# Performance work log

Hardware: AMD Instinct MI355X
Metric: run time of the kernel (lower is better)

The kernel has to match this reference:

```python
import jax, jax.numpy as jnp
import numpy as np

NUM_ITERS = 10
G_KSIZE, G_SIGMA = 5, 0.5
BIL_KSIZE, BIL_SIG_COLOR, BIL_SIG_SPACE = 5, 0.5, 5.0
EDGE_KSIZE, EDGE_SIG_COLOR, EDGE_SIG_SPACE = 5, 0.5, 5.0


def _gauss1d(ksize, sigma):
    x = jnp.arange(ksize, dtype=jnp.float32) - ksize // 2  # odd ksize -> centered (kornia)
    g = jnp.exp(-(x * x) / (2.0 * sigma * sigma))
    return g / g.sum()


def gaussian_blur(q, ksize, sigma):
    # separable gaussian blur with reflect padding, kornia GaussianBlur2d semantics
    k = _gauss1d(ksize, sigma)
    r = ksize // 2
    B, C, H, W = q.shape
    qp = jnp.pad(q, ((0, 0), (0, 0), (r, r), (0, 0)), mode='reflect')
    q = sum(k[i] * qp[:, :, i:i + H, :] for i in range(ksize))
    qp = jnp.pad(q, ((0, 0), (0, 0), (0, 0), (r, r)), mode='reflect')
    q = sum(k[i] * qp[:, :, :, i:i + W] for i in range(ksize))
    return q


def bilateral_weights(guide, ksize, sigma_color, sigma_space):
    # kornia joint_bilateral_blur weights (l1 color distance, reflect border).
    # guide: [B, Cg, H, W] -> weights [B, K*K, H, W]; guidance is constant across
    # CRF iterations so we precompute the kernel once.
    B, Cg, H, W = guide.shape
    r = ksize // 2
    g1 = _gauss1d(ksize, sigma_space)
    space = jnp.outer(g1, g1)  # normalized 2d gaussian (kornia get_gaussian_kernel2d)
    gp = jnp.pad(guide, ((0, 0), (0, 0), (r, r), (r, r)), mode='reflect')
    inv2sc2 = -0.5 / (sigma_color * sigma_color)
    ws = []
    for dy in range(ksize):
        for dx in range(ksize):
            d = jnp.abs(gp[:, :, dy:dy + H, dx:dx + W] - guide).sum(axis=1)  # [B,H,W]
            ws.append(space[dy, dx] * jnp.exp(inv2sc2 * d * d))
    return jnp.stack(ws, axis=1)  # [B, K*K, H, W]


def bilateral_apply(q, weights, ksize):
    # q: [B,C,H,W], weights: [B,K*K,H,W]
    B, C, H, W = q.shape
    r = ksize // 2
    qp = jnp.pad(q, ((0, 0), (0, 0), (r, r), (r, r)), mode='reflect')
    num = jnp.zeros_like(q)
    idx = 0
    for dy in range(ksize):
        for dx in range(ksize):
            num = num + weights[:, idx][:, None] * qp[:, :, dy:dy + H, dx:dx + W]
            idx += 1
    den = weights.sum(axis=1)[:, None]  # [B,1,H,W]
    return num / den


def _compat(f):
    # compat matrix is -1 off-diagonal, 0 on diagonal:
    # pairwise[c] = -sum_{c'!=c} f[c'] = f[c] - sum_{c'} f[c']
    return f - f.sum(axis=1, keepdims=True)


def setup_inputs() -> dict:
    key = jax.random.key(0)
    k1, k2, k3 = jax.random.split(key, 3)
    B, C, H, W = 2, 21, 512, 512
    unary_logits = jax.random.normal(k1, (B, C, H, W), dtype=jnp.float32)
    image = jax.random.uniform(k2, (B, 3, H, W), dtype=jnp.float32)
    edges = jax.random.uniform(k3, (B, H, W), dtype=jnp.float32)
    return {"unary_logits": unary_logits, "image": image, "edges": edges}


def reference(unary_logits, image, edges):
    edges4 = edges[:, None]  # [B,1,H,W]
    w_rgb = bilateral_weights(image, BIL_KSIZE, BIL_SIG_COLOR, BIL_SIG_SPACE)
    w_edge = bilateral_weights(edges4, EDGE_KSIZE, EDGE_SIG_COLOR, EDGE_SIG_SPACE)
    q = jax.nn.softmax(unary_logits, axis=1)
    for _ in range(NUM_ITERS):
        sf = gaussian_blur(q, G_KSIZE, G_SIGMA)
        rf = bilateral_apply(q, w_rgb, BIL_KSIZE)
        ef = bilateral_apply(q, w_edge, EDGE_KSIZE)
        pairwise = _compat(sf) + _compat(rf) + _compat(ef)
        q = jax.nn.softmax(unary_logits - pairwise, axis=1)
    return q
```

## Files before the change

### kernel.cpp

```cpp
#include <hip/hip_runtime.h>
#include <math.h>

#define BATCH 2
#define NCH 21
#define CPAD 24
#define WUPAD 48
#define HH 512
#define WW 512
#define KS 5
#define RAD 2
#define NTAPS 25
#define NUM_ITERS 10

#define TXW 32
#define TYW 16
#define HXW (TXW + 2*RAD)
#define HYW (TYW + 2*RAD)
#define HPXW (HXW * HYW)

#define TW 32
#define TH 16
#define NTHR 512
#define SX 40
#define SY 24
#define SPX (SX * SY)
#define SCHUNK (SPX * 3)
#define EX 36
#define EY 20
#define EPX (EX * EY)
#define RING (EPX - TW*TH)

typedef _Float16 f16;
typedef _Float16 half8 __attribute__((ext_vector_type(8)));
typedef _Float16 half2v __attribute__((ext_vector_type(2)));

__device__ __forceinline__ int refl(int i, int n) {
    if (i < 0) i = -i;
    if (i >= n) i = 2*n - 2 - i;
    return i;
}

#define WSEL(h0, h1, h2, hl, t) \
    ((t) < 8 ? (h0)[(t)] : (t) < 16 ? (h1)[(t) - 8] : (t) < 24 ? (h2)[(t) - 16] : (hl))

__global__ __launch_bounds__(512) void setup_kernel(const float* __restrict__ image,
                                                    const float* __restrict__ edges,
                                                    const float* __restrict__ unary,
                                                    f16* __restrict__ wu,
                                                    f16* __restrict__ q) {
    __shared__ __align__(16) float4 spx[HYW][HXW];

    const int tx = threadIdx.x;
    const int ty = threadIdx.y;
    const int tid = ty * TXW + tx;
    const int x0 = blockIdx.x * TXW;
    const int y0 = blockIdx.y * TYW;
    const int b = blockIdx.z;
    const int x = x0 + tx;
    const int y = y0 + ty;
    const size_t plane = (size_t)HH * WW;
    const float* img = image + (size_t)b * 3 * plane;
    const float* edg = edges + (size_t)b * plane;

    for (int i = tid; i < HPXW; i += TXW * TYW) {
        int ly = i / HXW, lx = i - ly * HXW;
        int gy = refl(y0 + ly - RAD, HH);
        int gx = refl(x0 + lx - RAD, WW);
        int g = gy * WW + gx;
        float4 v;
        v.x = img[g];
        v.y = img[plane + g];
        v.z = img[2 * plane + g];
        v.w = edg[g];
        spx[ly][lx] = v;
    }

    float l[NCH];
    {
        const float* u = unary + (size_t)b * NCH * plane + (size_t)y * WW + x;
#pragma unroll
        for (int c = 0; c < NCH; c++) l[c] = u[c * plane];
    }

    __syncthreads();

    float gs[3];
    gs[0] = 1.0f; gs[1] = __expf(-1.0f / 50.0f); gs[2] = __expf(-4.0f / 50.0f);
    float gb[3];
    gb[0] = 1.0f; gb[1] = __expf(-2.0f); gb[2] = __expf(-8.0f);
    float gbs = gb[0] + 2.0f * (gb[1] + gb[2]);
    gb[0] /= gbs; gb[1] /= gbs; gb[2] /= gbs;

    const float4 c0 = spx[ty + RAD][tx + RAD];
    const float r0 = c0.x, g0 = c0.y, b0 = c0.z, e0 = c0.w;

    float wr[NTAPS], we[NTAPS];
    float sr = 0.f, se = 0.f;
#pragma unroll
    for (int dy = 0; dy < KS; dy++) {
#pragma unroll
        for (int dx = 0; dx < KS; dx++) {
            float sp = gs[abs(dy - RAD)] * gs[abs(dx - RAD)];
            float4 v = spx[ty + dy][tx + dx];
            float d = fabsf(v.x - r0)
                    + fabsf(v.y - g0)
                    + fabsf(v.z - b0);
            float w1 = sp * __expf(-2.0f * d * d);
            float de = fabsf(v.w - e0);
            float w2 = sp * __expf(-2.0f * de * de);
            wr[dy * KS + dx] = w1;
            we[dy * KS + dx] = w2;
            sr += w1;
            se += w2;
        }
    }
    float isr = 1.0f / sr, ise = 1.0f / se;
    float wt[NTAPS];
#pragma unroll
    for (int t = 0; t < NTAPS; t++) {
        int dy = t / KS, dx = t % KS;
        float g2 = gb[abs(dy - RAD)] * gb[abs(dx - RAD)];
        wt[t] = g2 + wr[t] * isr + we[t] * ise;
    }
    const size_t pixoff = (size_t)b * plane + (size_t)y * WW + x;

    {
        half8* wo = (half8*)(wu + pixoff * WUPAD);
        half8 v;
#pragma unroll
        for (int k = 0; k < 8; k++) v[k] = (f16)wt[k];
        wo[0] = v;
#pragma unroll
        for (int k = 0; k < 8; k++) v[k] = (f16)wt[8 + k];
        wo[1] = v;
#pragma unroll
        for (int k = 0; k < 8; k++) v[k] = (f16)wt[16 + k];
        wo[2] = v;
#pragma unroll
        for (int k = 0; k < 8; k++) v[k] = (f16)l[k];
        wo[3] = v;
#pragma unroll
        for (int k = 0; k < 8; k++) v[k] = (f16)l[8 + k];
        wo[4] = v;
#pragma unroll
        for (int k = 0; k < 5; k++) v[k] = (f16)l[16 + k];
        v[5] = (f16)wt[24];
        v[6] = (f16)0.f; v[7] = (f16)0.f;
        wo[5] = v;
    }

    {
        float m = l[0];
#pragma unroll
        for (int c = 1; c < NCH; c++) m = fmaxf(m, l[c]);
        float e[NCH];
        float s = 0.f;
#pragma unroll
        for (int c = 0; c < NCH; c++) { e[c] = __expf(l[c] - m); s += e[c]; }
        float is = 1.0f / s;
        half8* qo = (half8*)(q + pixoff * CPAD);
        half8 v;
#pragma unroll
        for (int k = 0; k < 8; k++) v[k] = (f16)(e[k] * is);
        qo[0] = v;
#pragma unroll
        for (int k = 0; k < 8; k++) v[k] = (f16)(e[8 + k] * is);
        qo[1] = v;
#pragma unroll
        for (int k = 0; k < 5; k++) v[k] = (f16)(e[16 + k] * is);
        v[5] = (f16)0.f; v[6] = (f16)0.f; v[7] = (f16)0.f;
        qo[2] = v;
    }
}

#define CONV_ACC_PK(acc2, lds, row0, col0, stride, W0, W1, W2, WL)                     \
    {                                                                                  \
        _Pragma("unroll")                                                              \
        for (int dy = 0; dy < KS; dy++) {                                              \
            _Pragma("unroll")                                                          \
            for (int dx = 0; dx < KS; dx++) {                                          \
                const f16 wt_ = WSEL(W0, W1, W2, WL, dy * KS + dx);                    \
                const half2v wv_ = {wt_, wt_};                                         \
                const f16* tp = (lds) + ((size_t)((row0) + dy) * (stride) + (col0) + dx) * CPAD; \
                half8 v0 = *(const half8*)(tp);                                        \
                half8 v1 = *(const half8*)(tp + 8);                                    \
                half8 v2 = *(const half8*)(tp + 16);                                   \
                acc2[0]  = __builtin_elementwise_fma(wv_, __builtin_shufflevector(v0, v0, 0, 1), acc2[0]);  \
                acc2[1]  = __builtin_elementwise_fma(wv_, __builtin_shufflevector(v0, v0, 2, 3), acc2[1]);  \
                acc2[2]  = __builtin_elementwise_fma(wv_, __builtin_shufflevector(v0, v0, 4, 5), acc2[2]);  \
                acc2[3]  = __builtin_elementwise_fma(wv_, __builtin_shufflevector(v0, v0, 6, 7), acc2[3]);  \
                acc2[4]  = __builtin_elementwise_fma(wv_, __builtin_shufflevector(v1, v1, 0, 1), acc2[4]);  \
                acc2[5]  = __builtin_elementwise_fma(wv_, __builtin_shufflevector(v1, v1, 2, 3), acc2[5]);  \
                acc2[6]  = __builtin_elementwise_fma(wv_, __builtin_shufflevector(v1, v1, 4, 5), acc2[6]);  \
                acc2[7]  = __builtin_elementwise_fma(wv_, __builtin_shufflevector(v1, v1, 6, 7), acc2[7]);  \
                acc2[8]  = __builtin_elementwise_fma(wv_, __builtin_shufflevector(v2, v2, 0, 1), acc2[8]);  \
                acc2[9]  = __builtin_elementwise_fma(wv_, __builtin_shufflevector(v2, v2, 2, 3), acc2[9]);  \
                acc2[10] = __builtin_elementwise_fma(wv_, __builtin_shufflevector(v2, v2, 4, 5), acc2[10]); \
            }                                                                          \
        }                                                                              \
    }

#define LOGITS_FROM_PK(l, acc2, U0, U1, U2)                                            \
    {                                                                                  \
        _Pragma("unroll")                                                              \
        for (int j = 0; j < 10; j++) {                                                 \
            l[2 * j]     = -(float)acc2[j][0];                                         \
            l[2 * j + 1] = -(float)acc2[j][1];                                         \
        }                                                                              \
        l[20] = -(float)acc2[10][0];                                                   \
        _Pragma("unroll")                                                              \
        for (int k = 0; k < 8; k++) l[k] += (float)U0[k];                              \
        _Pragma("unroll")                                                              \
        for (int k = 0; k < 8; k++) l[8 + k] += (float)U1[k];                          \
        _Pragma("unroll")                                                              \
        for (int k = 0; k < 5; k++) l[16 + k] += (float)U2[k];                         \
    }

template <bool FINAL>
__global__ __launch_bounds__(NTHR, 4) void crf_pair_kernel(const f16* __restrict__ qin,
                                                           const f16* __restrict__ wu,
                                                           void* __restrict__ qout) {
    __shared__ __align__(16) f16 buf[SPX][CPAD];

    const int tid = threadIdx.x;
    const int ix = tid & (TW - 1);
    const int iy = tid >> 5;

    const int flat = blockIdx.x;
    const int band = flat & 7;
    const int within = flat >> 3;
    const int b = within >> 6;
    const int r = within & 63;
    const int x0 = (r & 15) * TW;
    const int y0 = (band * 4 + (r >> 4)) * TH;
    const int gx = x0 + ix;
    const int gy = y0 + iy;
    const size_t plane = (size_t)HH * WW;

    const f16* qbase = qin + (size_t)b * plane * CPAD;
    f16* lbase = &buf[0][0];
    for (int idx = tid; idx < SCHUNK; idx += NTHR) {
        int px = idx / 3, h4 = idx - px * 3;
        int sly = px / SX, slx = px - sly * SX;
        int qy = refl(y0 - 4 + sly, HH);
        int qx = refl(x0 - 4 + slx, WW);
        const f16* g = qbase + ((size_t)(qy * WW + qx)) * CPAD + h4 * 8;
        __builtin_amdgcn_global_load_lds(
            (const __attribute__((address_space(1))) void*)g,
            (__attribute__((address_space(3))) void*)(lbase + (size_t)idx * 8),
            16, 0, 0);
    }

    const size_t pixoff = (size_t)b * plane + (size_t)gy * WW + gx;
    const half8* wp = (const half8*)(wu + pixoff * WUPAD);
    half8 wa0 = wp[0], wa1 = wp[1], wa2 = wp[2];
    half8 ui0 = wp[3], ui1 = wp[4], ui2 = wp[5];
    f16 wl = ui2[5];

    const bool has_ring = tid < RING;
    int rly = 0, rlx = 0;
    half8 wr0 = {}, wr1 = {}, wr2 = {}, ur0 = {}, ur1 = {}, ur2 = {};
    f16 wrl = (f16)0.f;
    if (has_ring) {
        int t = tid;
        if (t < 72)       { rly = t / 36;       rlx = t % 36; }
        else if (t < 144) { t -= 72;  rly = 18 + t / 36; rlx = t % 36; }
        else              { t -= 144; rly = 2 + (t >> 2); int c = t & 3; rlx = (c < 2) ? c : (c + 32); }
        int rgy = y0 + rly - 2, rgx = x0 + rlx - 2;
        int cy = min(max(rgy, 0), HH - 1);
        int cx = min(max(rgx, 0), WW - 1);
        size_t rpo = (size_t)b * plane + (size_t)cy * WW + cx;
        const half8* wpr = (const half8*)(wu + rpo * WUPAD);
        wr0 = wpr[0]; wr1 = wpr[1]; wr2 = wpr[2];
        ur0 = wpr[3]; ur1 = wpr[4]; ur2 = wpr[5];
        wrl = ur2[5];
    }

    __syncthreads();

    half8 qr0, qr1, qr2;
    if (has_ring) {
        half2v acc2[11];
#pragma unroll
        for (int j = 0; j < 11; j++) acc2[j] = (half2v){(f16)0.f, (f16)0.f};
        CONV_ACC_PK(acc2, lbase, rly, rlx, SX, wr0, wr1, wr2, wrl);
        float l[NCH];
        LOGITS_FROM_PK(l, acc2, ur0, ur1, ur2);
        float m = l[0];
#pragma unroll
        for (int c = 1; c < NCH; c++) m = fmaxf(m, l[c]);
        float s = 0.f;
#pragma unroll
        for (int c = 0; c < NCH; c++) { l[c] = __expf(l[c] - m); s += l[c]; }
        float is = 1.0f / s;
#pragma unroll
        for (int k = 0; k < 8; k++) qr0[k] = (f16)(l[k] * is);
#pragma unroll
        for (int k = 0; k < 8; k++) qr1[k] = (f16)(l[8 + k] * is);
#pragma unroll
        for (int k = 0; k < 5; k++) qr2[k] = (f16)(l[16 + k] * is);
        qr2[5] = (f16)0.f; qr2[6] = (f16)0.f; qr2[7] = (f16)0.f;
    }

    half8 qi0, qi1, qi2;
    {
        half2v acc2[11];
#pragma unroll
        for (int j = 0; j < 11; j++) acc2[j] = (half2v){(f16)0.f, (f16)0.f};
        CONV_ACC_PK(acc2, lbase, iy + 2, ix + 2, SX, wa0, wa1, wa2, wl);
        float l[NCH];
        LOGITS_FROM_PK(l, acc2, ui0, ui1, ui2);
        float m = l[0];
#pragma unroll
        for (int c = 1; c < NCH; c++) m = fmaxf(m, l[c]);
        float s = 0.f;
#pragma unroll
        for (int c = 0; c < NCH; c++) { l[c] = __expf(l[c] - m); s += l[c]; }
        float is = 1.0f / s;
#pragma unroll
        for (int k = 0; k < 8; k++) qi0[k] = (f16)(l[k] * is);
#pragma unroll
        for (int k = 0; k < 8; k++) qi1[k] = (f16)(l[8 + k] * is);
#pragma unroll
        for (int k = 0; k < 5; k++) qi2[k] = (f16)(l[16 + k] * is);
        qi2[5] = (f16)0.f; qi2[6] = (f16)0.f; qi2[7] = (f16)0.f;
    }

    __syncthreads();

    {
        half8* d = (half8*)(lbase + ((size_t)(iy + 2) * EX + (ix + 2)) * CPAD);
        d[0] = qi0; d[1] = qi1; d[2] = qi2;
        if (has_ring) {
            half8* dr = (half8*)(lbase + ((size_t)rly * EX + rlx) * CPAD);
            dr[0] = qr0; dr[1] = qr1; dr[2] = qr2;
        }
    }

    __syncthreads();

    {
        int ry[KS], rx[KS];
#pragma unroll
        for (int d = 0; d < KS; d++) {
            ry[d] = refl(gy + d - 2, HH) - (y0 - 2);
            rx[d] = refl(gx + d - 2, WW) - (x0 - 2);
        }
        half2v acc2[11];
#pragma unroll
        for (int j = 0; j < 11; j++) acc2[j] = (half2v){(f16)0.f, (f16)0.f};
#pragma unroll
        for (int dy = 0; dy < KS; dy++) {
#pragma unroll
            for (int dx = 0; dx < KS; dx++) {
                const f16 wt_ = WSEL(wa0, wa1, wa2, wl, dy * KS + dx);
                const half2v wv_ = {wt_, wt_};
                const f16* tp = lbase + ((size_t)ry[dy] * EX + rx[dx]) * CPAD;
                half8 v0 = *(const half8*)(tp);
                half8 v1 = *(const half8*)(tp + 8);
                half8 v2 = *(const half8*)(tp + 16);
                acc2[0]  = __builtin_elementwise_fma(wv_, __builtin_shufflevector(v0, v0, 0, 1), acc2[0]);
                acc2[1]  = __builtin_elementwise_fma(wv_, __builtin_shufflevector(v0, v0, 2, 3), acc2[1]);
                acc2[2]  = __builtin_elementwise_fma(wv_, __builtin_shufflevector(v0, v0, 4, 5), acc2[2]);
                acc2[3]  = __builtin_elementwise_fma(wv_, __builtin_shufflevector(v0, v0, 6, 7), acc2[3]);
                acc2[4]  = __builtin_elementwise_fma(wv_, __builtin_shufflevector(v1, v1, 0, 1), acc2[4]);
                acc2[5]  = __builtin_elementwise_fma(wv_, __builtin_shufflevector(v1, v1, 2, 3), acc2[5]);
                acc2[6]  = __builtin_elementwise_fma(wv_, __builtin_shufflevector(v1, v1, 4, 5), acc2[6]);
                acc2[7]  = __builtin_elementwise_fma(wv_, __builtin_shufflevector(v1, v1, 6, 7), acc2[7]);
                acc2[8]  = __builtin_elementwise_fma(wv_, __builtin_shufflevector(v2, v2, 0, 1), acc2[8]);
                acc2[9]  = __builtin_elementwise_fma(wv_, __builtin_shufflevector(v2, v2, 2, 3), acc2[9]);
                acc2[10] = __builtin_elementwise_fma(wv_, __builtin_shufflevector(v2, v2, 4, 5), acc2[10]);
            }
        }
        float l[NCH];
        LOGITS_FROM_PK(l, acc2, ui0, ui1, ui2);
        float m = l[0];
#pragma unroll
        for (int c = 1; c < NCH; c++) m = fmaxf(m, l[c]);
        float s = 0.f;
#pragma unroll
        for (int c = 0; c < NCH; c++) { l[c] = __expf(l[c] - m); s += l[c]; }
        float is = 1.0f / s;

        if (FINAL) {
            float* qo = (float*)qout + (size_t)b * NCH * plane + (size_t)gy * WW + gx;
#pragma unroll
            for (int c = 0; c < NCH; c++) qo[c * plane] = l[c] * is;
        } else {
            half8* qo = (half8*)((f16*)qout + pixoff * CPAD);
            half8 o0, o1, o2;
#pragma unroll
            for (int k = 0; k < 8; k++) o0[k] = (f16)(l[k] * is);
#pragma unroll
            for (int k = 0; k < 8; k++) o1[k] = (f16)(l[8 + k] * is);
#pragma unroll
            for (int k = 0; k < 5; k++) o2[k] = (f16)(l[16 + k] * is);
            o2[5] = (f16)0.f; o2[6] = (f16)0.f; o2[7] = (f16)0.f;
            qo[0] = o0; qo[1] = o1; qo[2] = o2;
        }
    }
}

extern "C" void kernel_launch(void* const* d_in, const int* in_sizes, int n_in,
                              void* d_out, int out_size, void* d_ws, size_t ws_size,
                              hipStream_t stream) {
    const float* unary = (const float*)d_in[0];
    const float* image = (const float*)d_in[1];
    const float* edges = (const float*)d_in[2];
    float* out = (float*)d_out;

    const size_t plane = (size_t)HH * WW;
    char* ws = (char*)d_ws;
    f16* wu = (f16*)ws;
    char* p1 = ws + sizeof(f16) * BATCH * plane * WUPAD;
    f16* qA = (f16*)p1;
    f16* qB = qA + (size_t)BATCH * plane * CPAD;

    dim3 gridW(WW / TXW, HH / TYW, BATCH);
    dim3 blockW(TXW, TYW, 1);
    setup_kernel<<<gridW, blockW, 0, stream>>>(image, edges, unary, wu, qA);

    const int nblk = (WW / TW) * (HH / TH) * BATCH;
    f16* qa = qA;
    f16* qb = qB;
    const int npairs = NUM_ITERS / 2;
    for (int it = 0; it < npairs - 1; it++) {
        crf_pair_kernel<false><<<nblk, NTHR, 0, stream>>>(qa, wu, (void*)qb);
        f16* t = qa; qa = qb; qb = t;
    }
    crf_pair_kernel<true><<<nblk, NTHR, 0, stream>>>(qa, wu, (void*)out);
}
```

Baseline: 284.6 us.

## Add dedicated ring warps so halo softmax runs alongside inner pixels

The fused two-iteration kernel grows from 512 to 640 threads per block. The extra two warps compute the halo-ring pixels, two per thread, while the original 512 threads only compute their inner pixel. Before, the first 208 threads did the ring pixel and then their inner pixel serially. This removes that imbalance at the cost of more threads per block and a lower occupancy bound (3 blocks per CU instead of 4).

```diff
diff --git a/kernel.cpp b/kernel.cpp
--- a/kernel.cpp
+++ b/kernel.cpp
@@ -20,7 +20,8 @@
 
 #define TW 32
 #define TH 16
-#define NTHR 512
+#define NTHR 640
+#define NINNER 512
 #define SX 40
 #define SY 24
 #define SPX (SX * SY)
@@ -38,6 +39,12 @@
     if (i < 0) i = -i;
     if (i >= n) i = 2*n - 2 - i;
     return i;
+}
+
+__device__ __forceinline__ void ring_map(int t, int& rly, int& rlx) {
+    if (t < 72)       { rly = t / 36;            rlx = t % 36; }
+    else if (t < 144) { t -= 72;  rly = 18 + t / 36; rlx = t % 36; }
+    else              { t -= 144; rly = 2 + (t >> 2); int c = t & 3; rlx = (c < 2) ? c : (c + 32); }
 }
 
 #define WSEL(h0, h1, h2, hl, t) \
@@ -216,8 +223,32 @@
         for (int k = 0; k < 5; k++) l[16 + k] += (float)U2[k];                         \
     }
 
+#define CONV_SOFTMAX(o0, o1, o2, row0, col0, W0, W1, W2, WL, U0, U1, U2)               \
+    {                                                                                  \
+        half2v acc2[11];                                                               \
+        _Pragma("unroll")                                                              \
+        for (int j = 0; j < 11; j++) acc2[j] = (half2v){(f16)0.f, (f16)0.f};           \
+        CONV_ACC_PK(acc2, lbase, row0, col0, SX, W0, W1, W2, WL);                      \
+        float l_[NCH];                                                                 \
+        LOGITS_FROM_PK(l_, acc2, U0, U1, U2);                                          \
+        float m_ = l_[0];                                                              \
+        _Pragma("unroll")                                                              \
+        for (int c = 1; c < NCH; c++) m_ = fmaxf(m_, l_[c]);                           \
+        float s_ = 0.f;                                                                \
+        _Pragma("unroll")                                                              \
+        for (int c = 0; c < NCH; c++) { l_[c] = __expf(l_[c] - m_); s_ += l_[c]; }     \
+        float is_ = 1.0f / s_;                                                         \
+        _Pragma("unroll")                                                              \
+        for (int k = 0; k < 8; k++) (o0)[k] = (f16)(l_[k] * is_);                      \
+        _Pragma("unroll")                                                              \
+        for (int k = 0; k < 8; k++) (o1)[k] = (f16)(l_[8 + k] * is_);                  \
+        _Pragma("unroll")                                                              \
+        for (int k = 0; k < 5; k++) (o2)[k] = (f16)(l_[16 + k] * is_);                 \
+        (o2)[5] = (f16)0.f; (o2)[6] = (f16)0.f; (o2)[7] = (f16)0.f;                    \
+    }
+
 template <bool FINAL>
-__global__ __launch_bounds__(NTHR, 4) void crf_pair_kernel(const f16* __restrict__ qin,
+__global__ __launch_bounds__(NTHR, 3) void crf_pair_kernel(const f16* __restrict__ qin,
                                                            const f16* __restrict__ wu,
                                                            void* __restrict__ qout) {
     __shared__ __align__(16) f16 buf[SPX][CPAD];
@@ -225,6 +256,7 @@
     const int tid = threadIdx.x;
     const int ix = tid & (TW - 1);
     const int iy = tid >> 5;
+    const bool is_inner = tid < NINNER;
 
     const int flat = blockIdx.x;
     const int band = flat & 7;
@@ -252,94 +284,78 @@
     }
 
     const size_t pixoff = (size_t)b * plane + (size_t)gy * WW + gx;
-    const half8* wp = (const half8*)(wu + pixoff * WUPAD);
-    half8 wa0 = wp[0], wa1 = wp[1], wa2 = wp[2];
-    half8 ui0 = wp[3], ui1 = wp[4], ui2 = wp[5];
-    f16 wl = ui2[5];
-
-    const bool has_ring = tid < RING;
-    int rly = 0, rlx = 0;
-    half8 wr0 = {}, wr1 = {}, wr2 = {}, ur0 = {}, ur1 = {}, ur2 = {};
-    f16 wrl = (f16)0.f;
-    if (has_ring) {
-        int t = tid;
-        if (t < 72)       { rly = t / 36;       rlx = t % 36; }
-        else if (t < 144) { t -= 72;  rly = 18 + t / 36; rlx = t % 36; }
-        else              { t -= 144; rly = 2 + (t >> 2); int c = t & 3; rlx = (c < 2) ? c : (c + 32); }
-        int rgy = y0 + rly - 2, rgx = x0 + rlx - 2;
-        int cy = min(max(rgy, 0), HH - 1);
-        int cx = min(max(rgx, 0), WW - 1);
-        size_t rpo = (size_t)b * plane + (size_t)cy * WW + cx;
-        const half8* wpr = (const half8*)(wu + rpo * WUPAD);
-        wr0 = wpr[0]; wr1 = wpr[1]; wr2 = wpr[2];
-        ur0 = wpr[3]; ur1 = wpr[4]; ur2 = wpr[5];
-        wrl = ur2[5];
+    half8 wa0 = {}, wa1 = {}, wa2 = {}, ui0 = {}, ui1 = {}, ui2 = {};
+    f16 wl = (f16)0.f;
+    if (is_inner) {
+        const half8* wp = (const half8*)(wu + pixoff * WUPAD);
+        wa0 = wp[0]; wa1 = wp[1]; wa2 = wp[2];
+        ui0 = wp[3]; ui1 = wp[4]; ui2 = wp[5];
+        wl = ui2[5];
+    }
+
+    int rlyA = 0, rlxA = 0, rlyB = 0, rlxB = 0;
+    bool has_rB = false;
+    half8 wrA0 = {}, wrA1 = {}, wrA2 = {}, urA0 = {}, urA1 = {}, urA2 = {};
+    half8 wrB0 = {}, wrB1 = {}, wrB2 = {}, urB0 = {}, urB1 = {}, urB2 = {};
+    f16 wrlA = (f16)0.f, wrlB = (f16)0.f;
+    if (!is_inner) {
+        int j = tid - NINNER;
+        ring_map(j, rlyA, rlxA);
+        {
+            int rgy = y0 + rlyA - 2, rgx = x0 + rlxA - 2;
+            int cy = min(max(rgy, 0), HH - 1);
+            int cx = min(max(rgx, 0), WW - 1);
+            size_t rpo = (size_t)b * plane + (size_t)cy * WW + cx;
+            const half8* wpr = (const half8*)(wu + rpo * WUPAD);
+            wrA0 = wpr[0]; wrA1 = wpr[1]; wrA2 = wpr[2];
+            urA0 = wpr[3]; urA1 = wpr[4]; urA2 = wpr[5];
+            wrlA = urA2[5];
+        }
+        has_rB = (j < RING - 128);
+        if (has_rB) {
+            ring_map(128 + j, rlyB, rlxB);
+            int rgy = y0 + rlyB - 2, rgx = x0 + rlxB - 2;
+            int cy = min(max(rgy, 0), HH - 1);
+            int cx = min(max(rgx, 0), WW - 1);
+            size_t rpo = (size_t)b * plane + (size_t)cy * WW + cx;
+            const half8* wpr = (const half8*)(wu + rpo * WUPAD);
+            wrB0 = wpr[0]; wrB1 = wpr[1]; wrB2 = wpr[2];
+            urB0 = wpr[3]; urB1 = wpr[4]; urB2 = wpr[5];
+            wrlB = urB2[5];
+        }
     }
 
     __syncthreads();
 
-    half8 qr0, qr1, qr2;
-    if (has_ring) {
-        half2v acc2[11];
-#pragma unroll
-        for (int j = 0; j < 11; j++) acc2[j] = (half2v){(f16)0.f, (f16)0.f};
-        CONV_ACC_PK(acc2, lbase, rly, rlx, SX, wr0, wr1, wr2, wrl);
-        float l[NCH];
-        LOGITS_FROM_PK(l, acc2, ur0, ur1, ur2);
-        float m = l[0];
-#pragma unroll
-        for (int c = 1; c < NCH; c++) m = fmaxf(m, l[c]);
-        float s = 0.f;
-#pragma unroll
-        for (int c = 0; c < NCH; c++) { l[c] = __expf(l[c] - m); s += l[c]; }
-        float is = 1.0f / s;
-#pragma unroll
-        for (int k = 0; k < 8; k++) qr0[k] = (f16)(l[k] * is);
-#pragma unroll
-        for (int k = 0; k < 8; k++) qr1[k] = (f16)(l[8 + k] * is);
-#pragma unroll
-        for (int k = 0; k < 5; k++) qr2[k] = (f16)(l[16 + k] * is);
-        qr2[5] = (f16)0.f; qr2[6] = (f16)0.f; qr2[7] = (f16)0.f;
-    }
-
     half8 qi0, qi1, qi2;
-    {
-        half2v acc2[11];
-#pragma unroll
-        for (int j = 0; j < 11; j++) acc2[j] = (half2v){(f16)0.f, (f16)0.f};
-        CONV_ACC_PK(acc2, lbase, iy + 2, ix + 2, SX, wa0, wa1, wa2, wl);
-        float l[NCH];
-        LOGITS_FROM_PK(l, acc2, ui0, ui1, ui2);
-        float m = l[0];
-#pragma unroll
-        for (int c = 1; c < NCH; c++) m = fmaxf(m, l[c]);
-        float s = 0.f;
-#pragma unroll
-        for (int c = 0; c < NCH; c++) { l[c] = __expf(l[c] - m); s += l[c]; }
-        float is = 1.0f / s;
-#pragma unroll
-        for (int k = 0; k < 8; k++) qi0[k] = (f16)(l[k] * is);
-#pragma unroll
-        for (int k = 0; k < 8; k++) qi1[k] = (f16)(l[8 + k] * is);
-#pragma unroll
-        for (int k = 0; k < 5; k++) qi2[k] = (f16)(l[16 + k] * is);
-        qi2[5] = (f16)0.f; qi2[6] = (f16)0.f; qi2[7] = (f16)0.f;
+    half8 qa0, qa1, qa2;
+    half8 qb0, qb1, qb2;
+    if (is_inner) {
+        CONV_SOFTMAX(qi0, qi1, qi2, iy + 2, ix + 2, wa0, wa1, wa2, wl, ui0, ui1, ui2);
+    } else {
+        CONV_SOFTMAX(qa0, qa1, qa2, rlyA, rlxA, wrA0, wrA1, wrA2, wrlA, urA0, urA1, urA2);
+        if (has_rB) {
+            CONV_SOFTMAX(qb0, qb1, qb2, rlyB, rlxB, wrB0, wrB1, wrB2, wrlB, urB0, urB1, urB2);
+        }
     }
 
     __syncthreads();
 
-    {
+    if (is_inner) {
         half8* d = (half8*)(lbase + ((size_t)(iy + 2) * EX + (ix + 2)) * CPAD);
         d[0] = qi0; d[1] = qi1; d[2] = qi2;
-        if (has_ring) {
-            half8* dr = (half8*)(lbase + ((size_t)rly * EX + rlx) * CPAD);
-            dr[0] = qr0; dr[1] = qr1; dr[2] = qr2;
+    } else {
+        half8* dA = (half8*)(lbase + ((size_t)rlyA * EX + rlxA) * CPAD);
+        dA[0] = qa0; dA[1] = qa1; dA[2] = qa2;
+        if (has_rB) {
+            half8* dB = (half8*)(lbase + ((size_t)rlyB * EX + rlxB) * CPAD);
+            dB[0] = qb0; dB[1] = qb1; dB[2] = qb2;
         }
     }
 
     __syncthreads();
 
-    {
+    if (is_inner) {
         int ry[KS], rx[KS];
 #pragma unroll
         for (int d = 0; d < KS; d++) {
```

Measured after the change: 358.4 us. 25.9% more time.
